# Kernel optimization log

Measured on AMD Instinct MI355X. Metric: run time of the kernel, lower is better.

The kernel has to match this reference:

```python
import jax, jax.numpy as jnp
import numpy as np

EPS = 1e-5


def _ln(x, g, b):
    m = jnp.mean(x, axis=-1, keepdims=True)
    v = jnp.var(x, axis=-1, keepdims=True)
    return (x - m) * jax.lax.rsqrt(v + EPS) * g + b


def setup_inputs() -> dict:
    key = jax.random.key(0)
    B, N, C, H = 1, 384, 128, 128
    ks = jax.random.split(key, 8)

    def lin(k, fan_in, fan_out):
        return (jax.random.normal(k, (fan_in, fan_out), jnp.float32)
                / np.float32(np.sqrt(fan_in)))

    return {
        "pair": jax.random.normal(ks[0], (B, N, N, C), jnp.float32),
        # LayerNorm params
        "g_left": jnp.ones((C,), jnp.float32), "b_left": jnp.zeros((C,), jnp.float32),
        "g_right": jnp.ones((C,), jnp.float32), "b_right": jnp.zeros((C,), jnp.float32),
        "g_out": jnp.ones((C,), jnp.float32), "b_out": jnp.zeros((C,), jnp.float32),
        # Linear params (stored as (in, out))
        "W_l": lin(ks[1], C, H), "bias_l": jnp.zeros((H,), jnp.float32),
        "W_r": lin(ks[2], C, H), "bias_r": jnp.zeros((H,), jnp.float32),
        "W_g": lin(ks[3], C, H), "bias_g": jnp.zeros((H,), jnp.float32),
        "W_e": lin(ks[4], C, H), "bias_e": jnp.zeros((H,), jnp.float32),
        "W_o": lin(ks[5], H, C), "bias_o": jnp.zeros((C,), jnp.float32),
    }


def reference(pair, g_left, b_left, g_right, b_right, g_out, b_out,
              W_l, bias_l, W_r, bias_r, W_g, bias_g, W_e, bias_e,
              W_o, bias_o):
    # pair: (B, N, N, C)
    left = _ln(pair, g_left, b_left) @ W_l + bias_l        # (B,N,N,H)
    right = _ln(pair, g_right, b_right) @ W_r + bias_r     # (B,N,N,H)
    gate = jax.nn.sigmoid(pair @ W_g + bias_g)             # (B,N,N,H)
    left = left + pair @ W_e + bias_e                      # eq branch
    # triangular multiplication: contract over k per hidden channel
    out = jnp.einsum('bikh,bkjh->bijh', left, right)       # (B,N,N,H)
    out = out * gate
    out = out @ W_o + bias_o                               # (B,N,N,C)
    return _ln(out + pair, g_out, b_out)
```

## Files before the change

### kernel.cpp

```cpp
#include <hip/hip_runtime.h>

#define N_  384
#define C_  128
#define NN_ (N_*N_)

typedef __bf16 bf16x8 __attribute__((ext_vector_type(8)));
typedef float  floatx4 __attribute__((ext_vector_type(4)));

__device__ inline unsigned short f2bf(float f) {
    __bf16 h = (__bf16)f;
    return __builtin_bit_cast(unsigned short, h);
}

__global__ void prep(
    const float* __restrict__ Wl, const float* __restrict__ Wr,
    const float* __restrict__ Wg, const float* __restrict__ We,
    const float* __restrict__ gl, const float* __restrict__ bl,
    const float* __restrict__ gr, const float* __restrict__ br,
    const float* __restrict__ bsl, const float* __restrict__ bse,
    const float* __restrict__ bsr,
    __bf16* __restrict__ WtL, __bf16* __restrict__ WtE,
    __bf16* __restrict__ WtR, __bf16* __restrict__ WtG,
    float* __restrict__ cL, float* __restrict__ cR,
    float* __restrict__ sEw, float* __restrict__ sGw)
{
    const int b = blockIdx.x, t = threadIdx.x;
    if (b < 4) {
        const float* W  = (b==0) ? Wl  : (b==1) ? We  : (b==2) ? Wr  : Wg;
        __bf16*      Wt = (b==0) ? WtL : (b==1) ? WtE : (b==2) ? WtR : WtG;
        float scale = (b==0) ? gl[t] : (b==2) ? gr[t] : 1.f;
        for (int h = 0; h < C_; ++h)
            Wt[(size_t)h*C_ + t] = (__bf16)(W[(size_t)t*C_ + h] * scale);
    } else {
        float aL = 0.f, aR = 0.f, aE = 0.f, aG = 0.f;
        for (int c = 0; c < C_; ++c) {
            aL += bl[c] * Wl[(size_t)c*C_ + t];
            aR += br[c] * Wr[(size_t)c*C_ + t];
            aE += We[(size_t)c*C_ + t];
            aG += Wg[(size_t)c*C_ + t];
        }
        cL[t]  = aL + bsl[t] + bse[t];
        cR[t]  = aR + bsr[t];
        sEw[t] = aE;
        sGw[t] = aG;
    }
}

__global__ __launch_bounds__(256) void p_proj(
    const float* __restrict__ pair,
    const __bf16* __restrict__ WtL, const __bf16* __restrict__ WtE,
    const __bf16* __restrict__ WtR, const __bf16* __restrict__ WtG,
    const float* __restrict__ cL, const float* __restrict__ cR,
    const float* __restrict__ sEw, const float* __restrict__ sGw,
    const float* __restrict__ bsg,
    int h0,
    __bf16* __restrict__ leftC, __bf16* __restrict__ rightC,
    __bf16* __restrict__ gateC)
{
    __shared__ __align__(16) __bf16 sW4[4][32][128];
    __shared__ __align__(16) __bf16 sT3[3][32][72];
    __shared__ float sM[64], sIv[64];

    const int t = threadIdx.x;
    const int rid0 = blockIdx.x * 64;
    const int lane = t & 63, w = t >> 6;
    const int l15 = lane & 15, quad = lane >> 4;

    bf16x8 yf[4];
    {
        const int myrow = w*16 + l15;
        const float* prow = pair + (size_t)(rid0 + myrow)*C_;
        float4 xa[4], xb[4];
        float s = 0.f, sq = 0.f;
        #pragma unroll
        for (int ks = 0; ks < 4; ++ks) {
            xa[ks] = *(const float4*)(prow + ks*32 + quad*8);
            xb[ks] = *(const float4*)(prow + ks*32 + quad*8 + 4);
            s  += xa[ks].x + xa[ks].y + xa[ks].z + xa[ks].w
                + xb[ks].x + xb[ks].y + xb[ks].z + xb[ks].w;
            sq += xa[ks].x*xa[ks].x + xa[ks].y*xa[ks].y
                + xa[ks].z*xa[ks].z + xa[ks].w*xa[ks].w
                + xb[ks].x*xb[ks].x + xb[ks].y*xb[ks].y
                + xb[ks].z*xb[ks].z + xb[ks].w*xb[ks].w;
        }
        s  += __shfl_xor(s, 16);  s  += __shfl_xor(s, 32);
        sq += __shfl_xor(sq, 16); sq += __shfl_xor(sq, 32);
        float m  = s * (1.f/128.f);
        float v  = sq * (1.f/128.f) - m*m;
        float rs = rsqrtf(v + 1e-5f);
        if (quad == 0) { sM[myrow] = m; sIv[myrow] = 1.f / rs; }
        #pragma unroll
        for (int ks = 0; ks < 4; ++ks) {
            yf[ks][0] = (__bf16)((xa[ks].x - m)*rs);
            yf[ks][1] = (__bf16)((xa[ks].y - m)*rs);
            yf[ks][2] = (__bf16)((xa[ks].z - m)*rs);
            yf[ks][3] = (__bf16)((xa[ks].w - m)*rs);
            yf[ks][4] = (__bf16)((xb[ks].x - m)*rs);
            yf[ks][5] = (__bf16)((xb[ks].y - m)*rs);
            yf[ks][6] = (__bf16)((xb[ks].z - m)*rs);
            yf[ks][7] = (__bf16)((xb[ks].w - m)*rs);
        }
    }

    for (int half = 0; half < 2; ++half) {
        const int hb = h0 + half*32;
        {
            const int hh = t >> 3, c8 = t & 7;
            const __bf16* srcs[4] = {
                WtL + (size_t)(hb + hh)*C_, WtE + (size_t)(hb + hh)*C_,
                WtR + (size_t)(hb + hh)*C_, WtG + (size_t)(hb + hh)*C_ };
            #pragma unroll
            for (int mat = 0; mat < 4; ++mat) {
                #pragma unroll
                for (int rep = 0; rep < 2; ++rep) {
                    int cc = c8 + rep*8;
                    *(uint4*)&sW4[mat][hh][((cc ^ (hh & 7)) << 3)] =
                        *(const uint4*)(srcs[mat] + cc*8);
                }
            }
        }
        __syncthreads();

        floatx4 aL[2] = {}, aE[2] = {}, aR[2] = {}, aG[2] = {};
        #pragma unroll
        for (int ks = 0; ks < 4; ++ks) {
            const int cs = ((ks*4 + quad) ^ (l15 & 7)) << 3;
            const bf16x8 af = yf[ks];
            #pragma unroll
            for (int nt = 0; nt < 2; ++nt) {
                const int hr = nt*16 + l15;
                aL[nt] = __builtin_amdgcn_mfma_f32_16x16x32_bf16(
                    af, *(const bf16x8*)&sW4[0][hr][cs], aL[nt], 0, 0, 0);
                aE[nt] = __builtin_amdgcn_mfma_f32_16x16x32_bf16(
                    af, *(const bf16x8*)&sW4[1][hr][cs], aE[nt], 0, 0, 0);
                aR[nt] = __builtin_amdgcn_mfma_f32_16x16x32_bf16(
                    af, *(const bf16x8*)&sW4[2][hr][cs], aR[nt], 0, 0, 0);
                aG[nt] = __builtin_amdgcn_mfma_f32_16x16x32_bf16(
                    af, *(const bf16x8*)&sW4[3][hr][cs], aG[nt], 0, 0, 0);
            }
        }

        #pragma unroll
        for (int nt = 0; nt < 2; ++nt) {
            const int hl_ = nt*16 + l15;
            const float se = sEw[hb + hl_], clv = cL[hb + hl_];
            const float crv = cR[hb + hl_];
            const float sg_ = sGw[hb + hl_], bg = bsg[hb + hl_];
            #pragma unroll
            for (int reg = 0; reg < 4; ++reg) {
                const int rr = w*16 + quad*4 + reg;
                sT3[0][hl_][rr] = (__bf16)(aL[nt][reg] + sIv[rr]*aE[nt][reg]
                                           + sM[rr]*se + clv);
                sT3[1][hl_][rr] = (__bf16)(aR[nt][reg] + crv);
                float z = sIv[rr]*aG[nt][reg] + sM[rr]*sg_ + bg;
                sT3[2][hl_][rr] = (__bf16)(1.f / (1.f + expf(-z)));
            }
        }
        __syncthreads();
        {
            const int hh = t >> 3, sg = t & 7;
            const size_t off = (size_t)(half*32 + hh)*NN_ + rid0 + sg*8;
            *(uint4*)(leftC  + off) = *(const uint4*)&sT3[0][hh][sg*8];
            *(uint4*)(rightC + off) = *(const uint4*)&sT3[1][hh][sg*8];
            *(uint4*)(gateC  + off) = *(const uint4*)&sT3[2][hh][sg*8];
        }
        if (half == 0) __syncthreads();
    }
}

__global__ __launch_bounds__(256) void t_right(__bf16* __restrict__ p)
{
    __shared__ __align__(16) __bf16 tA[64][72];
    __shared__ __align__(16) __bf16 tB[64][72];
    const int plane = blockIdx.x / 21;
    int rem = blockIdx.x % 21, ri = 0;
    while (rem >= 6 - ri) { rem -= 6 - ri; ++ri; }
    const int ci = ri + rem;
    __bf16* base = p + (size_t)plane * NN_;
    const int t = threadIdx.x;
    const int r = t >> 2, c0 = (t & 3) * 16;

    {
        const __bf16* srcA = base + (size_t)(ri*64 + r)*N_ + ci*64 + c0;
        *(uint4*)&tA[r][c0]   = *(const uint4*)(srcA);
        *(uint4*)&tA[r][c0+8] = *(const uint4*)(srcA + 8);
        if (ri != ci) {
            const __bf16* srcB = base + (size_t)(ci*64 + r)*N_ + ri*64 + c0;
            *(uint4*)&tB[r][c0]   = *(const uint4*)(srcB);
            *(uint4*)&tB[r][c0+8] = *(const uint4*)(srcB + 8);
        }
    }
    __syncthreads();
    {
        union { unsigned short us[8]; uint4 v; } o0, o1;
        #pragma unroll
        for (int u = 0; u < 8; ++u) {
            o0.us[u] = __builtin_bit_cast(unsigned short, tA[c0+u][r]);
            o1.us[u] = __builtin_bit_cast(unsigned short, tA[c0+8+u][r]);
        }
        __bf16* dA = base + (size_t)(ci*64 + r)*N_ + ri*64 + c0;
        *(uint4*)(dA)     = o0.v;
        *(uint4*)(dA + 8) = o1.v;
        if (ri != ci) {
            union { unsigned short us[8]; uint4 v; } p0, p1;
            #pragma unroll
            for (int u = 0; u < 8; ++u) {
                p0.us[u] = __builtin_bit_cast(unsigned short, tB[c0+u][r]);
                p1.us[u] = __builtin_bit_cast(unsigned short, tB[c0+8+u][r]);
            }
            __bf16* dB = base + (size_t)(ri*64 + r)*N_ + ci*64 + c0;
            *(uint4*)(dB)     = p0.v;
            *(uint4*)(dB + 8) = p1.v;
        }
    }
}

__global__ __launch_bounds__(256) void k_einsum(
    const __bf16* __restrict__ leftC, const __bf16* __restrict__ rightC,
    const __bf16* __restrict__ gate, __bf16* __restrict__ outG)
{
    __shared__ __align__(16) unsigned char smem[128*136*2];
    __bf16 (*sA)[40]    = (__bf16(*)[40])smem;
    __bf16 (*sB)[40]    = (__bf16(*)[40])(smem + 128*40*2);
    __bf16 (*sGate)[136] = (__bf16(*)[136])smem;

    const int bid = (blockIdx.x & 7) * 72 + (blockIdx.x >> 3);
    const int hl = bid / 9, t9 = bid % 9;
    const int ti = (t9 / 3) * 128, tj = (t9 % 3) * 128;
    const int tid = threadIdx.x, lane = tid & 63, w = tid >> 6;
    const int l15 = lane & 15, quad = lane >> 4;
    const size_t hNN = (size_t)hl * NN_;

    const int ar = (lane >> 2);
    const int ac = (lane & 3) * 8;
    const __bf16* gA = leftC  + hNN + (size_t)ti * N_;
    const __bf16* gB = rightC + hNN + (size_t)tj * N_;

    floatx4 acc[4][4] = {};

    for (int ks = 0; ks < 12; ++ks) {
        const int kc = ks * 32;
        uint4 va[2], vb[2];
        #pragma unroll
        for (int it = 0; it < 2; ++it) {
            int row = w*32 + it*16 + ar;
            va[it] = *(const uint4*)(gA + (size_t)row*N_ + kc + ac);
            vb[it] = *(const uint4*)(gB + (size_t)row*N_ + kc + ac);
        }
        #pragma unroll
        for (int it = 0; it < 2; ++it) {
            int row = w*32 + it*16 + ar;
            *(uint4*)&sA[row][ac] = va[it];
            *(uint4*)&sB[row][ac] = vb[it];
        }
        __syncthreads();
        bf16x8 af[4], bfr[4];
        #pragma unroll
        for (int mt = 0; mt < 4; ++mt)
            af[mt] = *(const bf16x8*)&sA[(w&1)*64 + mt*16 + l15][quad*8];
        #pragma unroll
        for (int nt = 0; nt < 4; ++nt)
            bfr[nt] = *(const bf16x8*)&sB[(w>>1)*64 + nt*16 + l15][quad*8];
        #pragma unroll
        for (int mt = 0; mt < 4; ++mt)
            #pragma unroll
            for (int nt = 0; nt < 4; ++nt)
                acc[mt][nt] = __builtin_amdgcn_mfma_f32_16x16x32_bf16(
                    af[mt], bfr[nt], acc[mt][nt], 0, 0, 0);
        __syncthreads();
    }

    #pragma unroll
    for (int it = 0; it < 8; ++it) {
        int cid = it*256 + tid;
        int ri = cid >> 4, c8 = cid & 15;
        *(uint4*)&sGate[ri][c8*8] =
            *(const uint4*)(gate + hNN + (size_t)(ti + ri)*N_ + tj + c8*8);
    }
    __syncthreads();

    const int ib = (w & 1) * 64, jbw = (w >> 1) * 64;
    #pragma unroll
    for (int mt = 0; mt < 4; ++mt) {
        const int i_base = ib + mt*16 + quad*4;
        #pragma unroll
        for (int nt = 0; nt < 4; ++nt) {
            const int j_loc = jbw + nt*16 + l15;
            union { unsigned short us[4]; uint2 v; } p;
            #pragma unroll
            for (int rr = 0; rr < 4; ++rr) {
                float g = (float)sGate[i_base + rr][j_loc];
                p.us[rr] = f2bf(acc[mt][nt][rr] * g);
            }
            *(uint2*)(outG + hNN + (size_t)(tj + j_loc)*N_ + ti + i_base) = p.v;
        }
    }
}

__global__ __launch_bounds__(256) void p_out(
    const __bf16* __restrict__ outG, const float* __restrict__ Wo,
    const float* __restrict__ bso,  const float* __restrict__ pair,
    const float* __restrict__ go,   const float* __restrict__ bo,
    float* __restrict__ out)
{
    __shared__ __align__(16) __bf16 sOh[64][128];
    __shared__ __align__(16) __bf16 sWo[128][128];

    const int t = threadIdx.x;
    const int j  = blockIdx.x / 6;
    const int i0 = (blockIdx.x % 6) * 64;
    const int lane = t & 63, w = t >> 6;
    const int l15 = lane & 15, quad = lane >> 4;

    {
        const int h = t >> 1, ibase = (t & 1) * 32;
        const __bf16* src = outG + (size_t)h*NN_ + (size_t)j*N_ + i0 + ibase;
        #pragma unroll
        for (int u = 0; u < 4; ++u) {
            uint4 vv = *(const uint4*)(src + u*8);
            const unsigned short* pv = (const unsigned short*)&vv;
            #pragma unroll
            for (int k = 0; k < 8; ++k) {
                int i = ibase + u*8 + k;
                sOh[i][(((h >> 3) ^ (i & 7)) << 3) + (h & 7)] =
                    __builtin_bit_cast(__bf16, pv[k]);
            }
        }
    }
    {
        const int h = t >> 1, cbase = (t & 1) * 64;
        const float* src = Wo + (size_t)h*C_ + cbase;
        #pragma unroll
        for (int u = 0; u < 16; ++u) {
            float4 wv = *(const float4*)(src + u*4);
            const float* wf = (const float*)&wv;
            #pragma unroll
            for (int k = 0; k < 4; ++k) {
                int c = cbase + u*4 + k;
                sWo[c][(((h >> 3) ^ (c & 7)) << 3) + (h & 7)] = (__bf16)wf[k];
            }
        }
    }
    __syncthreads();

    floatx4 acc[8] = {};
    #pragma unroll
    for (int ks = 0; ks < 4; ++ks) {
        const int cs = ((ks*4 + quad) ^ (l15 & 7)) << 3;
        bf16x8 af = *(const bf16x8*)&sOh[w*16 + l15][cs];
        #pragma unroll
        for (int nt = 0; nt < 8; ++nt)
            acc[nt] = __builtin_amdgcn_mfma_f32_16x16x32_bf16(
                af, *(const bf16x8*)&sWo[nt*16 + l15][cs], acc[nt], 0, 0, 0);
    }

    float bsov[8], gov[8], bov[8];
    #pragma unroll
    for (int nt = 0; nt < 8; ++nt) {
        const int c = nt*16 + l15;
        bsov[nt] = bso[c]; gov[nt] = go[c]; bov[nt] = bo[c];
    }

    #pragma unroll
    for (int reg = 0; reg < 4; ++reg) {
        const int i = i0 + w*16 + quad*4 + reg;
        const float* prow = pair + ((size_t)i*N_ + j)*C_;
        float zz[8];
        float ssum = 0.f, ssq = 0.f;
        #pragma unroll
        for (int nt = 0; nt < 8; ++nt) {
            float zv = acc[nt][reg] + bsov[nt] + prow[nt*16 + l15];
            zz[nt] = zv; ssum += zv; ssq += zv*zv;
        }
        #pragma unroll
        for (int d = 1; d < 16; d <<= 1) {
            ssum += __shfl_xor(ssum, d);
            ssq  += __shfl_xor(ssq, d);
        }
        const float mm = ssum * (1.f/128.f);
        const float vv = ssq * (1.f/128.f) - mm*mm;
        const float rr = rsqrtf(vv + 1e-5f);
        float* orow = out + ((size_t)i*N_ + j)*C_;
        #pragma unroll
        for (int nt = 0; nt < 8; ++nt)
            orow[nt*16 + l15] = (zz[nt] - mm)*rr*gov[nt] + bov[nt];
    }
}

extern "C" void kernel_launch(void* const* d_in, const int* in_sizes, int n_in,
                              void* d_out, int out_size, void* d_ws, size_t ws_size,
                              hipStream_t stream)
{
    const float* pair    = (const float*)d_in[0];
    const float* g_left  = (const float*)d_in[1];
    const float* b_left  = (const float*)d_in[2];
    const float* g_right = (const float*)d_in[3];
    const float* b_right = (const float*)d_in[4];
    const float* g_out   = (const float*)d_in[5];
    const float* b_out   = (const float*)d_in[6];
    const float* W_l     = (const float*)d_in[7];
    const float* bias_l  = (const float*)d_in[8];
    const float* W_r     = (const float*)d_in[9];
    const float* bias_r  = (const float*)d_in[10];
    const float* W_g     = (const float*)d_in[11];
    const float* bias_g  = (const float*)d_in[12];
    const float* W_e     = (const float*)d_in[13];
    const float* bias_e  = (const float*)d_in[14];
    const float* W_o     = (const float*)d_in[15];
    const float* bias_o  = (const float*)d_in[16];

    __bf16* outG   = (__bf16*)d_ws;
    __bf16* leftC  = (__bf16*)d_out;
    __bf16* rightC = leftC + (size_t)64*NN_;
    __bf16* gateC  = leftC + (size_t)128*NN_;

    char* prepBase = (char*)d_out + ((size_t)60 << 20);
    __bf16* WtL = (__bf16*)prepBase;
    __bf16* WtE = WtL + 16384;
    __bf16* WtR = WtL + 32768;
    __bf16* WtG = WtL + 49152;
    float*  cL  = (float*)(WtL + 65536);
    float*  cR  = cL + 128;
    float*  sEw = cL + 256;
    float*  sGw = cL + 384;

    prep<<<5, 128, 0, stream>>>(W_l, W_r, W_g, W_e,
                                g_left, b_left, g_right, b_right,
                                bias_l, bias_e, bias_r,
                                WtL, WtE, WtR, WtG, cL, cR, sEw, sGw);

    for (int h0 = 0; h0 < 128; h0 += 64) {
        p_proj<<<NN_/64, 256, 0, stream>>>(pair, WtL, WtE, WtR, WtG,
                                           cL, cR, sEw, sGw, bias_g,
                                           h0, leftC, rightC, gateC);
        t_right<<<64*21, 256, 0, stream>>>(rightC);
        k_einsum<<<64*9, 256, 0, stream>>>(leftC, rightC, gateC,
                                           outG + (size_t)h0*NN_);
    }
    p_out<<<2304, 256, 0, stream>>>(outG, W_o, bias_o, pair, g_out, b_out,
                                    (float*)d_out);
}
```

Measured before the change: 326.8 us.

## Process all hidden channels in one pass when workspace allows

Adds a path used when the workspace is large enough: right-projection and einsum outputs move to the workspace, so p_proj computes all 128 hidden channels in a single launch (nh=4). t_right and k_einsum then each run once over all 128 planes. This avoids reading the pair tensor and recomputing its LayerNorm twice, and halves the number of kernel launches. The price is a larger workspace requirement; the old two-pass path stays as a fallback.

```diff
diff --git a/kernel.cpp b/kernel.cpp
--- a/kernel.cpp
+++ b/kernel.cpp
@@ -53,7 +53,7 @@
     const float* __restrict__ cL, const float* __restrict__ cR,
     const float* __restrict__ sEw, const float* __restrict__ sGw,
     const float* __restrict__ bsg,
-    int h0,
+    int h0, int nh,
     __bf16* __restrict__ leftC, __bf16* __restrict__ rightC,
     __bf16* __restrict__ gateC)
 {
@@ -102,7 +102,7 @@
         }
     }
 
-    for (int half = 0; half < 2; ++half) {
+    for (int half = 0; half < nh; ++half) {
         const int hb = h0 + half*32;
         {
             const int hh = t >> 3, c8 = t & 7;
@@ -164,7 +164,7 @@
             *(uint4*)(rightC + off) = *(const uint4*)&sT3[1][hh][sg*8];
             *(uint4*)(gateC  + off) = *(const uint4*)&sT3[2][hh][sg*8];
         }
-        if (half == 0) __syncthreads();
+        if (half + 1 < nh) __syncthreads();
     }
 }
 
@@ -224,7 +224,8 @@
     __bf16 (*sB)[40]    = (__bf16(*)[40])(smem + 128*40*2);
     __bf16 (*sGate)[136] = (__bf16(*)[136])smem;
 
-    const int bid = (blockIdx.x & 7) * 72 + (blockIdx.x >> 3);
+    const int cpx = gridDim.x >> 3;
+    const int bid = (blockIdx.x & 7) * cpx + (blockIdx.x >> 3);
     const int hl = bid / 9, t9 = bid % 9;
     const int ti = (t9 / 3) * 128, tj = (t9 % 3) * 128;
     const int tid = threadIdx.x, lane = tid & 63, w = tid >> 6;
@@ -409,34 +410,65 @@
     const float* W_o     = (const float*)d_in[15];
     const float* bias_o  = (const float*)d_in[16];
 
-    __bf16* outG   = (__bf16*)d_ws;
-    __bf16* leftC  = (__bf16*)d_out;
-    __bf16* rightC = leftC + (size_t)64*NN_;
-    __bf16* gateC  = leftC + (size_t)128*NN_;
-
-    char* prepBase = (char*)d_out + ((size_t)60 << 20);
-    __bf16* WtL = (__bf16*)prepBase;
-    __bf16* WtE = WtL + 16384;
-    __bf16* WtR = WtL + 32768;
-    __bf16* WtG = WtL + 49152;
-    float*  cL  = (float*)(WtL + 65536);
-    float*  cR  = cL + 128;
-    float*  sEw = cL + 256;
-    float*  sGw = cL + 384;
-
-    prep<<<5, 128, 0, stream>>>(W_l, W_r, W_g, W_e,
-                                g_left, b_left, g_right, b_right,
-                                bias_l, bias_e, bias_r,
-                                WtL, WtE, WtR, WtG, cL, cR, sEw, sGw);
-
-    for (int h0 = 0; h0 < 128; h0 += 64) {
+    const size_t PLANES128 = (size_t)128 * NN_;
+    const size_t NEED = PLANES128*2*2 + 65536*2 + 512*4;
+
+    if (ws_size >= NEED) {
+        __bf16* leftC  = (__bf16*)d_out;
+        __bf16* gateC  = leftC + PLANES128;
+        __bf16* rightC = (__bf16*)d_ws;
+        __bf16* outG   = rightC + PLANES128;
+        char* prepBase = (char*)d_ws + PLANES128*2*2;
+        __bf16* WtL = (__bf16*)prepBase;
+        __bf16* WtE = WtL + 16384;
+        __bf16* WtR = WtL + 32768;
+        __bf16* WtG = WtL + 49152;
+        float*  cL  = (float*)(WtL + 65536);
+        float*  cR  = cL + 128;
+        float*  sEw = cL + 256;
+        float*  sGw = cL + 384;
+
+        prep<<<5, 128, 0, stream>>>(W_l, W_r, W_g, W_e,
+                                    g_left, b_left, g_right, b_right,
+                                    bias_l, bias_e, bias_r,
+                                    WtL, WtE, WtR, WtG, cL, cR, sEw, sGw);
         p_proj<<<NN_/64, 256, 0, stream>>>(pair, WtL, WtE, WtR, WtG,
                                            cL, cR, sEw, sGw, bias_g,
-                                           h0, leftC, rightC, gateC);
-        t_right<<<64*21, 256, 0, stream>>>(rightC);
-        k_einsum<<<64*9, 256, 0, stream>>>(leftC, rightC, gateC,
-                                           outG + (size_t)h0*NN_);
-    }
-    p_out<<<2304, 256, 0, stream>>>(outG, W_o, bias_o, pair, g_out, b_out,
-                                    (float*)d_out);
-}
+                                           0, 4, leftC, rightC, gateC);
+        t_right<<<128*21, 256, 0, stream>>>(rightC);
+        k_einsum<<<128*9, 256, 0, stream>>>(leftC, rightC, gateC, outG);
+        p_out<<<2304, 256, 0, stream>>>(outG, W_o, bias_o, pair,
+                                        g_out, b_out, (float*)d_out);
+    } else {
+        __bf16* outG   = (__bf16*)d_ws;
+        __bf16* leftC  = (__bf16*)d_out;
+        __bf16* rightC = leftC + (size_t)64*NN_;
+        __bf16* gateC  = leftC + (size_t)128*NN_;
+
+        char* prepBase = (char*)d_out + ((size_t)60 << 20);
+        __bf16* WtL = (__bf16*)prepBase;
+        __bf16* WtE = WtL + 16384;
+        __bf16* WtR = WtL + 32768;
+        __bf16* WtG = WtL + 49152;
+        float*  cL  = (float*)(WtL + 65536);
+        float*  cR  = cL + 128;
+        float*  sEw = cL + 256;
+        float*  sGw = cL + 384;
+
+        prep<<<5, 128, 0, stream>>>(W_l, W_r, W_g, W_e,
+                                    g_left, b_left, g_right, b_right,
+                                    bias_l, bias_e, bias_r,
+                                    WtL, WtE, WtR, WtG, cL, cR, sEw, sGw);
+
+        for (int h0 = 0; h0 < 128; h0 += 64) {
+            p_proj<<<NN_/64, 256, 0, stream>>>(pair, WtL, WtE, WtR, WtG,
+                                               cL, cR, sEw, sGw, bias_g,
+                                               h0, 2, leftC, rightC, gateC);
+            t_right<<<64*21, 256, 0, stream>>>(rightC);
+            k_einsum<<<64*9, 256, 0, stream>>>(leftC, rightC, gateC,
+                                               outG + (size_t)h0*NN_);
+        }
+        p_out<<<2304, 256, 0, stream>>>(outG, W_o, bias_o, pair,
+                                        g_out, b_out, (float*)d_out);
+    }
+}
```

New measurement: 293.8 us. 1.11x faster.
